# Optimization experiments

Hardware: AMD Instinct MI355X
Metric: run time of the kernel (lower is better)

Reference implementation:

```python
import jax, jax.numpy as jnp
import numpy as np

D_MODEL = 1024


def setup_inputs() -> dict:
    key = jax.random.key(0)
    ks = jax.random.split(key, 7)
    d = D_MODEL
    x = jax.random.normal(ks[0], (4, 2048, d), dtype=jnp.float32)
    scale = 1.0 / np.sqrt(d)
    Wq = jax.random.normal(ks[1], (d, d), dtype=jnp.float32) * scale
    bq = jax.random.normal(ks[2], (d,), dtype=jnp.float32) * 0.01
    Wk = jax.random.normal(ks[3], (d, d), dtype=jnp.float32) * scale
    bk = jax.random.normal(ks[4], (d,), dtype=jnp.float32) * 0.01
    Wo = jax.random.normal(ks[5], (d, 1), dtype=jnp.float32) * scale
    bo = jax.random.normal(ks[6], (1,), dtype=jnp.float32) * 0.01
    return {"x": x, "Wq": Wq, "bq": bq, "Wk": Wk, "bk": bk, "Wo": Wo, "bo": bo}


def reference(x, Wq, bq, Wk, bk, Wo, bo):
    # x: [B, N, d]
    Q = x @ Wq + bq                      # [B, N, d]
    K = x @ Wk + bk                      # [B, N, d]
    scale = x.shape[-1] ** (-0.5)
    content_logits = jnp.einsum('bnd,bmd->bnm', Q, K) * scale  # [B, N, N]
    s = (x @ Wo + bo)[..., 0]            # [B, N]
    # ordering_bias[b, i, j] = tanh(s[b, j] - s[b, i]) * 5
    ordering_bias = jnp.tanh(s[:, None, :] - s[:, :, None]) * 5.0
    return content_logits + ordering_bias
```

## Files before the change

kernel.cpp:

```cpp
#include <hip/hip_runtime.h>
#include <math.h>

#define D_MODEL 1024
#define SEQ 2048
#define NBATCH 4

using bf16x8 = __attribute__((ext_vector_type(8))) short;
using f32x4  = __attribute__((ext_vector_type(4))) float;

__device__ __forceinline__ unsigned short f2bf(float f) {
  union { float f; unsigned int u; } v; v.f = f;
  return (unsigned short)((v.u + 0x7fffu + ((v.u >> 16) & 1u)) >> 16);
}

__device__ __forceinline__ void async_cp16(const void* g, void* l) {
  __builtin_amdgcn_global_load_lds(
      (const __attribute__((address_space(1))) void*)g,
      (__attribute__((address_space(3))) void*)l, 16, 0, 0);
}

__global__ __launch_bounds__(256) void prep_x_kernel(
    const float* __restrict__ x, const float* __restrict__ Wo,
    const float* __restrict__ bo, unsigned short* __restrict__ xb,
    float* __restrict__ tb) {
  const int m = blockIdx.x;
  const int tid = threadIdx.x;
  const float4 xv = ((const float4*)(x + (size_t)m * D_MODEL))[tid];
  const float4 wv = ((const float4*)Wo)[tid];
  ushort4 o;
  o.x = f2bf(xv.x); o.y = f2bf(xv.y); o.z = f2bf(xv.z); o.w = f2bf(xv.w);
  ((ushort4*)(xb + (size_t)m * D_MODEL))[tid] = o;
  float p = xv.x * wv.x + xv.y * wv.y + xv.z * wv.z + xv.w * wv.w;
  #pragma unroll
  for (int off = 32; off > 0; off >>= 1) p += __shfl_down(p, off, 64);
  __shared__ float red[4];
  if ((tid & 63) == 0) red[tid >> 6] = p;
  __syncthreads();
  if (tid == 0) {
    float s = red[0] + red[1] + red[2] + red[3] + bo[0];
    tb[m] = tanhf(s);
  }
}

__global__ __launch_bounds__(256) void prep_w_kernel(
    const float* __restrict__ Wq, const float* __restrict__ Wk,
    unsigned short* __restrict__ WqT, unsigned short* __restrict__ WkT) {
  const float* W = blockIdx.z ? Wk : Wq;
  unsigned short* WT = blockIdx.z ? WkT : WqT;
  const int k0 = blockIdx.y * 32, n0 = blockIdx.x * 32;
  __shared__ unsigned short lds[32][36];
  const int tid = threadIdx.x;
  const int r = tid >> 3, c = (tid & 7) * 4;
  float4 v = *(const float4*)(&W[(size_t)(k0 + r) * D_MODEL + n0 + c]);
  lds[r][c + 0] = f2bf(v.x); lds[r][c + 1] = f2bf(v.y);
  lds[r][c + 2] = f2bf(v.z); lds[r][c + 3] = f2bf(v.w);
  __syncthreads();
  ushort4 o;
  o.x = lds[c + 0][r]; o.y = lds[c + 1][r];
  o.z = lds[c + 2][r]; o.w = lds[c + 3][r];
  *(ushort4*)(&WT[(size_t)(n0 + r) * D_MODEL + k0 + c]) = o;
}

__global__ __launch_bounds__(256) void qkgen_kernel(
    const unsigned short* __restrict__ xb,
    const unsigned short* __restrict__ WqT,
    const unsigned short* __restrict__ WkT,
    const float* __restrict__ bq, const float* __restrict__ bk,
    unsigned short* __restrict__ Qb, unsigned short* __restrict__ Kb) {
  const unsigned short* Bt = blockIdx.z ? WkT : WqT;
  const float* bias = blockIdx.z ? bk : bq;
  unsigned short* Cout = blockIdx.z ? Kb : Qb;
  const int m0 = blockIdx.x * 128;
  const int n0 = blockIdx.y * 128;
  __shared__ unsigned short As[128 * 32];
  __shared__ unsigned short Bs[128 * 32];
  const int tid = threadIdx.x;
  const int lane = tid & 63, w = tid >> 6;
  const int wm = w >> 1, wn = w & 1;
  const int l16 = lane & 15, quad = lane >> 4;

  f32x4 acc[4][4];
  #pragma unroll
  for (int i = 0; i < 4; i++)
    #pragma unroll
    for (int j = 0; j < 4; j++) acc[i][j] = f32x4{0.f, 0.f, 0.f, 0.f};

  const int srow = tid >> 2;
  const int sseg = (tid & 3) * 8;
  const unsigned short* gA = xb + (size_t)(m0 + srow) * D_MODEL + sseg;
  const unsigned short* gB = Bt + (size_t)(n0 + srow) * D_MODEL + sseg;
  unsigned short* lA = As + tid * 8;
  unsigned short* lB = Bs + tid * 8;

  for (int k0 = 0; k0 < D_MODEL; k0 += 32) {
    async_cp16(gA + k0, lA);
    async_cp16(gA + k0 + (size_t)64 * D_MODEL, lA + 2048);
    async_cp16(gB + k0, lB);
    async_cp16(gB + k0 + (size_t)64 * D_MODEL, lB + 2048);
    __syncthreads();
    bf16x8 af[4], bfr[4];
    #pragma unroll
    for (int mt = 0; mt < 4; mt++)
      af[mt] = *(const bf16x8*)(As + (wm * 64 + mt * 16 + l16) * 32 + quad * 8);
    #pragma unroll
    for (int nt = 0; nt < 4; nt++)
      bfr[nt] = *(const bf16x8*)(Bs + (wn * 64 + nt * 16 + l16) * 32 + quad * 8);
    #pragma unroll
    for (int mt = 0; mt < 4; mt++)
      #pragma unroll
      for (int nt = 0; nt < 4; nt++)
        acc[mt][nt] = __builtin_amdgcn_mfma_f32_16x16x32_bf16(
            af[mt], bfr[nt], acc[mt][nt], 0, 0, 0);
    __syncthreads();
  }

  float bv[4];
  #pragma unroll
  for (int nt = 0; nt < 4; nt++) bv[nt] = bias[n0 + wn * 64 + nt * 16 + l16];
  #pragma unroll
  for (int mt = 0; mt < 4; mt++) {
    #pragma unroll
    for (int r = 0; r < 4; r++) {
      const int row = m0 + wm * 64 + mt * 16 + quad * 4 + r;
      unsigned short* cp = Cout + (size_t)row * D_MODEL + n0 + wn * 64 + l16;
      #pragma unroll
      for (int nt = 0; nt < 4; nt++)
        cp[nt * 16] = f2bf(acc[mt][nt][r] + bv[nt]);
    }
  }
}

__global__ __launch_bounds__(256) void qkt_kernel(
    const unsigned short* __restrict__ Qb,
    const unsigned short* __restrict__ Kb,
    const float* __restrict__ tb, float* __restrict__ out) {
  const int b = blockIdx.z;
  const int i0 = blockIdx.x * 128;
  const int j0 = blockIdx.y * 128;
  const unsigned short* A = Qb + (size_t)b * SEQ * D_MODEL;
  const unsigned short* Bt = Kb + (size_t)b * SEQ * D_MODEL;
  __shared__ unsigned short As[128 * 32];
  __shared__ unsigned short Bs[128 * 32];
  __shared__ float tsi[128], tsj[128];
  const int tid = threadIdx.x;
  if (tid < 128) tsi[tid] = tb[b * SEQ + i0 + tid];
  else           tsj[tid - 128] = tb[b * SEQ + j0 + tid - 128];
  const int lane = tid & 63, w = tid >> 6;
  const int wm = w >> 1, wn = w & 1;
  const int l16 = lane & 15, quad = lane >> 4;

  f32x4 acc[4][4];
  #pragma unroll
  for (int i = 0; i < 4; i++)
    #pragma unroll
    for (int j = 0; j < 4; j++) acc[i][j] = f32x4{0.f, 0.f, 0.f, 0.f};

  const int srow = tid >> 2;
  const int sseg = (tid & 3) * 8;
  const unsigned short* gA = A + (size_t)(i0 + srow) * D_MODEL + sseg;
  const unsigned short* gB = Bt + (size_t)(j0 + srow) * D_MODEL + sseg;
  unsigned short* lA = As + tid * 8;
  unsigned short* lB = Bs + tid * 8;

  for (int k0 = 0; k0 < D_MODEL; k0 += 32) {
    async_cp16(gA + k0, lA);
    async_cp16(gA + k0 + (size_t)64 * D_MODEL, lA + 2048);
    async_cp16(gB + k0, lB);
    async_cp16(gB + k0 + (size_t)64 * D_MODEL, lB + 2048);
    __syncthreads();
    bf16x8 af[4], bfr[4];
    #pragma unroll
    for (int mt = 0; mt < 4; mt++)
      af[mt] = *(const bf16x8*)(As + (wm * 64 + mt * 16 + l16) * 32 + quad * 8);
    #pragma unroll
    for (int nt = 0; nt < 4; nt++)
      bfr[nt] = *(const bf16x8*)(Bs + (wn * 64 + nt * 16 + l16) * 32 + quad * 8);
    #pragma unroll
    for (int mt = 0; mt < 4; mt++)
      #pragma unroll
      for (int nt = 0; nt < 4; nt++)
        acc[mt][nt] = __builtin_amdgcn_mfma_f32_16x16x32_bf16(
            af[mt], bfr[nt], acc[mt][nt], 0, 0, 0);
    __syncthreads();
  }

  float tj[4];
  #pragma unroll
  for (int nt = 0; nt < 4; nt++) tj[nt] = tsj[wn * 64 + nt * 16 + l16];
  #pragma unroll
  for (int mt = 0; mt < 4; mt++) {
    #pragma unroll
    for (int r = 0; r < 4; r++) {
      const int il = wm * 64 + mt * 16 + quad * 4 + r;
      const float ti = tsi[il];
      float* cp = out + ((size_t)(b * SEQ + i0 + il)) * SEQ + j0 + wn * 64 + l16;
      #pragma unroll
      for (int nt = 0; nt < 4; nt++) {
        const float num = tj[nt] - ti;
        const float den = fmaf(-tj[nt], ti, 1.0f);
        const float obias = 5.0f * num * __builtin_amdgcn_rcpf(den);
        cp[nt * 16] = 0.03125f * acc[mt][nt][r] + obias;
      }
    }
  }
}

extern "C" void kernel_launch(void* const* d_in, const int* in_sizes, int n_in,
                              void* d_out, int out_size, void* d_ws, size_t ws_size,
                              hipStream_t stream) {
  const float* x  = (const float*)d_in[0];
  const float* Wq = (const float*)d_in[1];
  const float* bq = (const float*)d_in[2];
  const float* Wk = (const float*)d_in[3];
  const float* bk = (const float*)d_in[4];
  const float* Wo = (const float*)d_in[5];
  const float* bo = (const float*)d_in[6];
  float* out = (float*)d_out;

  char* ws = (char*)d_ws;
  unsigned short* xb  = (unsigned short*)(ws);
  unsigned short* WqT = (unsigned short*)(ws + (16ull << 20));
  unsigned short* WkT = (unsigned short*)(ws + (18ull << 20));
  unsigned short* Qb  = (unsigned short*)(ws + (20ull << 20));
  unsigned short* Kb  = (unsigned short*)(ws + (36ull << 20));
  float*          tb  = (float*)(ws + (52ull << 20));

  prep_x_kernel<<<8192, 256, 0, stream>>>(x, Wo, bo, xb, tb);
  prep_w_kernel<<<dim3(32, 32, 2), 256, 0, stream>>>(Wq, Wk, WqT, WkT);
  qkgen_kernel<<<dim3(64, 8, 2), 256, 0, stream>>>(xb, WqT, WkT, bq, bk, Qb, Kb);
  qkt_kernel<<<dim3(16, 16, 4), 256, 0, stream>>>(Qb, Kb, tb, out);
}
```

Before: 203.8 us.

## Double-buffer LDS tiles with k-major layout in both GEMM kernels

```diff
diff --git a/kernel.cpp b/kernel.cpp
--- a/kernel.cpp
+++ b/kernel.cpp
@@ -17,6 +17,16 @@
   __builtin_amdgcn_global_load_lds(
       (const __attribute__((address_space(1))) void*)g,
       (__attribute__((address_space(3))) void*)l, 16, 0, 0);
+}
+
+__device__ __forceinline__ void stage_tile(const unsigned short* gA,
+                                           const unsigned short* gB,
+                                           unsigned short* As,
+                                           unsigned short* Bs, int tid) {
+  async_cp16(gA,      As + tid * 8);
+  async_cp16(gA + 16, As + tid * 8 + 2048);
+  async_cp16(gB,      Bs + tid * 8);
+  async_cp16(gB + 16, Bs + tid * 8 + 2048);
 }
 
 __global__ __launch_bounds__(256) void prep_x_kernel(
@@ -61,7 +71,7 @@
   *(ushort4*)(&WT[(size_t)(n0 + r) * D_MODEL + k0 + c]) = o;
 }
 
-__global__ __launch_bounds__(256) void qkgen_kernel(
+__global__ __launch_bounds__(256, 3) void qkgen_kernel(
     const unsigned short* __restrict__ xb,
     const unsigned short* __restrict__ WqT,
     const unsigned short* __restrict__ WkT,
@@ -72,8 +82,8 @@
   unsigned short* Cout = blockIdx.z ? Kb : Qb;
   const int m0 = blockIdx.x * 128;
   const int n0 = blockIdx.y * 128;
-  __shared__ unsigned short As[128 * 32];
-  __shared__ unsigned short Bs[128 * 32];
+  __shared__ unsigned short As[2][4096];
+  __shared__ unsigned short Bs[2][4096];
   const int tid = threadIdx.x;
   const int lane = tid & 63, w = tid >> 6;
   const int wm = w >> 1, wn = w & 1;
@@ -85,26 +95,27 @@
     #pragma unroll
     for (int j = 0; j < 4; j++) acc[i][j] = f32x4{0.f, 0.f, 0.f, 0.f};
 
-  const int srow = tid >> 2;
-  const int sseg = (tid & 3) * 8;
-  const unsigned short* gA = xb + (size_t)(m0 + srow) * D_MODEL + sseg;
-  const unsigned short* gB = Bt + (size_t)(n0 + srow) * D_MODEL + sseg;
-  unsigned short* lA = As + tid * 8;
-  unsigned short* lB = Bs + tid * 8;
-
-  for (int k0 = 0; k0 < D_MODEL; k0 += 32) {
-    async_cp16(gA + k0, lA);
-    async_cp16(gA + k0 + (size_t)64 * D_MODEL, lA + 2048);
-    async_cp16(gB + k0, lB);
-    async_cp16(gB + k0 + (size_t)64 * D_MODEL, lB + 2048);
-    __syncthreads();
+  const int strow = (w & 1) * 64 + lane;
+  const int stseg = (w >> 1) * 8;
+  const unsigned short* gA = xb + (size_t)(m0 + strow) * D_MODEL + stseg;
+  const unsigned short* gB = Bt + (size_t)(n0 + strow) * D_MODEL + stseg;
+
+  stage_tile(gA, gB, As[0], Bs[0], tid);
+  __syncthreads();
+
+  #pragma unroll 2
+  for (int kk = 0; kk < 32; ++kk) {
+    const int cur = kk & 1;
+    if (kk < 31)
+      stage_tile(gA + (kk + 1) * 32, gB + (kk + 1) * 32,
+                 As[cur ^ 1], Bs[cur ^ 1], tid);
     bf16x8 af[4], bfr[4];
     #pragma unroll
     for (int mt = 0; mt < 4; mt++)
-      af[mt] = *(const bf16x8*)(As + (wm * 64 + mt * 16 + l16) * 32 + quad * 8);
+      af[mt] = *(const bf16x8*)(&As[cur][quad * 1024 + (wm * 64 + mt * 16 + l16) * 8]);
     #pragma unroll
     for (int nt = 0; nt < 4; nt++)
-      bfr[nt] = *(const bf16x8*)(Bs + (wn * 64 + nt * 16 + l16) * 32 + quad * 8);
+      bfr[nt] = *(const bf16x8*)(&Bs[cur][quad * 1024 + (wn * 64 + nt * 16 + l16) * 8]);
     #pragma unroll
     for (int mt = 0; mt < 4; mt++)
       #pragma unroll
@@ -130,7 +141,7 @@
   }
 }
 
-__global__ __launch_bounds__(256) void qkt_kernel(
+__global__ __launch_bounds__(256, 3) void qkt_kernel(
     const unsigned short* __restrict__ Qb,
     const unsigned short* __restrict__ Kb,
     const float* __restrict__ tb, float* __restrict__ out) {
@@ -139,8 +150,8 @@
   const int j0 = blockIdx.y * 128;
   const unsigned short* A = Qb + (size_t)b * SEQ * D_MODEL;
   const unsigned short* Bt = Kb + (size_t)b * SEQ * D_MODEL;
-  __shared__ unsigned short As[128 * 32];
-  __shared__ unsigned short Bs[128 * 32];
+  __shared__ unsigned short As[2][4096];
+  __shared__ unsigned short Bs[2][4096];
   __shared__ float tsi[128], tsj[128];
   const int tid = threadIdx.x;
   if (tid < 128) tsi[tid] = tb[b * SEQ + i0 + tid];
@@ -155,26 +166,27 @@
     #pragma unroll
     for (int j = 0; j < 4; j++) acc[i][j] = f32x4{0.f, 0.f, 0.f, 0.f};
 
-  const int srow = tid >> 2;
-  const int sseg = (tid & 3) * 8;
-  const unsigned short* gA = A + (size_t)(i0 + srow) * D_MODEL + sseg;
-  const unsigned short* gB = Bt + (size_t)(j0 + srow) * D_MODEL + sseg;
-  unsigned short* lA = As + tid * 8;
-  unsigned short* lB = Bs + tid * 8;
-
-  for (int k0 = 0; k0 < D_MODEL; k0 += 32) {
-    async_cp16(gA + k0, lA);
-    async_cp16(gA + k0 + (size_t)64 * D_MODEL, lA + 2048);
-    async_cp16(gB + k0, lB);
-    async_cp16(gB + k0 + (size_t)64 * D_MODEL, lB + 2048);
-    __syncthreads();
+  const int strow = (w & 1) * 64 + lane;
+  const int stseg = (w >> 1) * 8;
+  const unsigned short* gA = A + (size_t)(i0 + strow) * D_MODEL + stseg;
+  const unsigned short* gB = Bt + (size_t)(j0 + strow) * D_MODEL + stseg;
+
+  stage_tile(gA, gB, As[0], Bs[0], tid);
+  __syncthreads();
+
+  #pragma unroll 2
+  for (int kk = 0; kk < 32; ++kk) {
+    const int cur = kk & 1;
+    if (kk < 31)
+      stage_tile(gA + (kk + 1) * 32, gB + (kk + 1) * 32,
+                 As[cur ^ 1], Bs[cur ^ 1], tid);
     bf16x8 af[4], bfr[4];
     #pragma unroll
     for (int mt = 0; mt < 4; mt++)
-      af[mt] = *(const bf16x8*)(As + (wm * 64 + mt * 16 + l16) * 32 + quad * 8);
+      af[mt] = *(const bf16x8*)(&As[cur][quad * 1024 + (wm * 64 + mt * 16 + l16) * 8]);
     #pragma unroll
     for (int nt = 0; nt < 4; nt++)
-      bfr[nt] = *(const bf16x8*)(Bs + (wn * 64 + nt * 16 + l16) * 32 + quad * 8);
+      bfr[nt] = *(const bf16x8*)(&Bs[cur][quad * 1024 + (wn * 64 + nt * 16 + l16) * 8]);
     #pragma unroll
     for (int mt = 0; mt < 4; mt++)
       #pragma unroll
```

Measured after the change: 241.5 us. +18.5%, slower.

## Reassociate QK^T via precomputed Wq·Wk^T and double-buffer swizzled GEMM tiles

Applied to the files above, without the earlier changes.

```diff
diff --git a/kernel.cpp b/kernel.cpp
--- a/kernel.cpp
+++ b/kernel.cpp
@@ -3,7 +3,7 @@
 
 #define D_MODEL 1024
 #define SEQ 2048
-#define NBATCH 4
+#define SCALE 0.03125f
 
 using bf16x8 = __attribute__((ext_vector_type(8))) short;
 using f32x4  = __attribute__((ext_vector_type(4))) float;
@@ -19,187 +19,230 @@
       (__attribute__((address_space(3))) void*)l, 16, 0, 0);
 }
 
-__global__ __launch_bounds__(256) void prep_x_kernel(
-    const float* __restrict__ x, const float* __restrict__ Wo,
-    const float* __restrict__ bo, unsigned short* __restrict__ xb,
-    float* __restrict__ tb) {
-  const int m = blockIdx.x;
-  const int tid = threadIdx.x;
-  const float4 xv = ((const float4*)(x + (size_t)m * D_MODEL))[tid];
-  const float4 wv = ((const float4*)Wo)[tid];
-  ushort4 o;
-  o.x = f2bf(xv.x); o.y = f2bf(xv.y); o.z = f2bf(xv.z); o.w = f2bf(xv.w);
-  ((ushort4*)(xb + (size_t)m * D_MODEL))[tid] = o;
-  float p = xv.x * wv.x + xv.y * wv.y + xv.z * wv.z + xv.w * wv.w;
-  #pragma unroll
-  for (int off = 32; off > 0; off >>= 1) p += __shfl_down(p, off, 64);
-  __shared__ float red[4];
-  if ((tid & 63) == 0) red[tid >> 6] = p;
-  __syncthreads();
-  if (tid == 0) {
-    float s = red[0] + red[1] + red[2] + red[3] + bo[0];
-    tb[m] = tanhf(s);
-  }
-}
-
-__global__ __launch_bounds__(256) void prep_w_kernel(
-    const float* __restrict__ Wq, const float* __restrict__ Wk,
-    unsigned short* __restrict__ WqT, unsigned short* __restrict__ WkT) {
-  const float* W = blockIdx.z ? Wk : Wq;
-  unsigned short* WT = blockIdx.z ? WkT : WqT;
-  const int k0 = blockIdx.y * 32, n0 = blockIdx.x * 32;
-  __shared__ unsigned short lds[32][36];
-  const int tid = threadIdx.x;
-  const int r = tid >> 3, c = (tid & 7) * 4;
-  float4 v = *(const float4*)(&W[(size_t)(k0 + r) * D_MODEL + n0 + c]);
-  lds[r][c + 0] = f2bf(v.x); lds[r][c + 1] = f2bf(v.y);
-  lds[r][c + 2] = f2bf(v.z); lds[r][c + 3] = f2bf(v.w);
-  __syncthreads();
-  ushort4 o;
-  o.x = lds[c + 0][r]; o.y = lds[c + 1][r];
-  o.z = lds[c + 2][r]; o.w = lds[c + 3][r];
-  *(ushort4*)(&WT[(size_t)(n0 + r) * D_MODEL + k0 + c]) = o;
-}
-
-__global__ __launch_bounds__(256) void qkgen_kernel(
-    const unsigned short* __restrict__ xb,
-    const unsigned short* __restrict__ WqT,
-    const unsigned short* __restrict__ WkT,
-    const float* __restrict__ bq, const float* __restrict__ bk,
-    unsigned short* __restrict__ Qb, unsigned short* __restrict__ Kb) {
-  const unsigned short* Bt = blockIdx.z ? WkT : WqT;
-  const float* bias = blockIdx.z ? bk : bq;
-  unsigned short* Cout = blockIdx.z ? Kb : Qb;
-  const int m0 = blockIdx.x * 128;
-  const int n0 = blockIdx.y * 128;
-  __shared__ unsigned short As[128 * 32];
-  __shared__ unsigned short Bs[128 * 32];
-  const int tid = threadIdx.x;
+__device__ __forceinline__ const unsigned short* stage_ptr(
+    const unsigned short* base, int row0, int ld, int tid) {
+  const int r0 = tid >> 2;
+  const int s0 = ((tid & 3) ^ ((r0 >> 1) & 3)) * 8;
+  return base + (size_t)(row0 + r0) * ld + s0;
+}
+
+__device__ __forceinline__ void gemm_core(
+    const unsigned short* __restrict__ gA, const unsigned short* __restrict__ gB,
+    int lda, int ldb, unsigned short* As, unsigned short* Bs, int tid,
+    f32x4 acc[4][4]) {
   const int lane = tid & 63, w = tid >> 6;
   const int wm = w >> 1, wn = w & 1;
   const int l16 = lane & 15, quad = lane >> 4;
 
-  f32x4 acc[4][4];
-  #pragma unroll
-  for (int i = 0; i < 4; i++)
-    #pragma unroll
-    for (int j = 0; j < 4; j++) acc[i][j] = f32x4{0.f, 0.f, 0.f, 0.f};
-
-  const int srow = tid >> 2;
-  const int sseg = (tid & 3) * 8;
-  const unsigned short* gA = xb + (size_t)(m0 + srow) * D_MODEL + sseg;
-  const unsigned short* gB = Bt + (size_t)(n0 + srow) * D_MODEL + sseg;
-  unsigned short* lA = As + tid * 8;
-  unsigned short* lB = Bs + tid * 8;
-
-  for (int k0 = 0; k0 < D_MODEL; k0 += 32) {
-    async_cp16(gA + k0, lA);
-    async_cp16(gA + k0 + (size_t)64 * D_MODEL, lA + 2048);
-    async_cp16(gB + k0, lB);
-    async_cp16(gB + k0 + (size_t)64 * D_MODEL, lB + 2048);
-    __syncthreads();
-    bf16x8 af[4], bfr[4];
-    #pragma unroll
-    for (int mt = 0; mt < 4; mt++)
-      af[mt] = *(const bf16x8*)(As + (wm * 64 + mt * 16 + l16) * 32 + quad * 8);
-    #pragma unroll
-    for (int nt = 0; nt < 4; nt++)
-      bfr[nt] = *(const bf16x8*)(Bs + (wn * 64 + nt * 16 + l16) * 32 + quad * 8);
+  async_cp16(gA,            As + tid * 8);
+  async_cp16(gA + 64 * lda, As + 2048 + tid * 8);
+  async_cp16(gB,            Bs + tid * 8);
+  async_cp16(gB + 64 * ldb, Bs + 2048 + tid * 8);
+  __syncthreads();
+
+  #pragma unroll 2
+  for (int kk = 0; kk < 32; ++kk) {
+    const int cur = (kk & 1) * 4096;
+    const int nxt = 4096 - cur;
+    if (kk < 31) {
+      const unsigned short* a = gA + (kk + 1) * 32;
+      const unsigned short* b = gB + (kk + 1) * 32;
+      async_cp16(a,            As + nxt + tid * 8);
+      async_cp16(a + 64 * lda, As + nxt + 2048 + tid * 8);
+      async_cp16(b,            Bs + nxt + tid * 8);
+      async_cp16(b + 64 * ldb, Bs + nxt + 2048 + tid * 8);
+    }
+    bf16x8 afr[4], bfr[4];
+    #pragma unroll
+    for (int mt = 0; mt < 4; mt++) {
+      const int R = wm * 64 + mt * 16 + l16;
+      afr[mt] = *(const bf16x8*)(As + cur + (R * 4 + (quad ^ ((R >> 1) & 3))) * 8);
+    }
+    #pragma unroll
+    for (int nt = 0; nt < 4; nt++) {
+      const int R = wn * 64 + nt * 16 + l16;
+      bfr[nt] = *(const bf16x8*)(Bs + cur + (R * 4 + (quad ^ ((R >> 1) & 3))) * 8);
+    }
     #pragma unroll
     for (int mt = 0; mt < 4; mt++)
       #pragma unroll
       for (int nt = 0; nt < 4; nt++)
         acc[mt][nt] = __builtin_amdgcn_mfma_f32_16x16x32_bf16(
-            af[mt], bfr[nt], acc[mt][nt], 0, 0, 0);
+            afr[mt], bfr[nt], acc[mt][nt], 0, 0, 0);
     __syncthreads();
   }
-
-  float bv[4];
-  #pragma unroll
-  for (int nt = 0; nt < 4; nt++) bv[nt] = bias[n0 + wn * 64 + nt * 16 + l16];
-  #pragma unroll
-  for (int mt = 0; mt < 4; mt++) {
-    #pragma unroll
-    for (int r = 0; r < 4; r++) {
-      const int row = m0 + wm * 64 + mt * 16 + quad * 4 + r;
-      unsigned short* cp = Cout + (size_t)row * D_MODEL + n0 + wn * 64 + l16;
-      #pragma unroll
-      for (int nt = 0; nt < 4; nt++)
-        cp[nt * 16] = f2bf(acc[mt][nt][r] + bv[nt]);
-    }
-  }
-}
-
-__global__ __launch_bounds__(256) void qkt_kernel(
-    const unsigned short* __restrict__ Qb,
-    const unsigned short* __restrict__ Kb,
-    const float* __restrict__ tb, float* __restrict__ out) {
-  const int b = blockIdx.z;
-  const int i0 = blockIdx.x * 128;
-  const int j0 = blockIdx.y * 128;
-  const unsigned short* A = Qb + (size_t)b * SEQ * D_MODEL;
-  const unsigned short* Bt = Kb + (size_t)b * SEQ * D_MODEL;
-  __shared__ unsigned short As[128 * 32];
-  __shared__ unsigned short Bs[128 * 32];
-  __shared__ float tsi[128], tsj[128];
-  const int tid = threadIdx.x;
-  if (tid < 128) tsi[tid] = tb[b * SEQ + i0 + tid];
-  else           tsj[tid - 128] = tb[b * SEQ + j0 + tid - 128];
+}
+
+__device__ __forceinline__ void store_c_bf16(f32x4 acc[4][4],
+                                             unsigned short* C, int ldc,
+                                             int m0, int n0, int tid) {
   const int lane = tid & 63, w = tid >> 6;
   const int wm = w >> 1, wn = w & 1;
   const int l16 = lane & 15, quad = lane >> 4;
-
+  #pragma unroll
+  for (int mt = 0; mt < 4; mt++) {
+    #pragma unroll
+    for (int r = 0; r < 4; r++) {
+      const int row = m0 + wm * 64 + mt * 16 + quad * 4 + r;
+      unsigned short* cp = C + (size_t)row * ldc + n0 + wn * 64 + l16;
+      #pragma unroll
+      for (int nt = 0; nt < 4; nt++) cp[nt * 16] = f2bf(acc[mt][nt][r]);
+    }
+  }
+}
+
+__global__ __launch_bounds__(256) void wcvt_kernel(
+    const float* __restrict__ Wq, const float* __restrict__ Wk,
+    const float* __restrict__ bq, const float* __restrict__ bk,
+    unsigned short* __restrict__ Wqb, unsigned short* __restrict__ Wkb,
+    float* __restrict__ u, float* __restrict__ v, float* __restrict__ sc) {
+  const int blk = blockIdx.x, tid = threadIdx.x;
+  __shared__ float red[4];
+  float p;
+  if (blk < 2048) {
+    const bool isq = blk < 1024;
+    const int row = blk & 1023;
+    const float* W = isq ? Wq : Wk;
+    const float* bias = isq ? bk : bq;
+    const float4 wv = ((const float4*)(W + (size_t)row * D_MODEL))[tid];
+    const float4 bv = ((const float4*)bias)[tid];
+    ushort4 o;
+    o.x = f2bf(wv.x); o.y = f2bf(wv.y); o.z = f2bf(wv.z); o.w = f2bf(wv.w);
+    ((ushort4*)((isq ? Wqb : Wkb) + (size_t)row * D_MODEL))[tid] = o;
+    p = wv.x * bv.x + wv.y * bv.y + wv.z * bv.z + wv.w * bv.w;
+    #pragma unroll
+    for (int off = 32; off > 0; off >>= 1) p += __shfl_down(p, off, 64);
+    if ((tid & 63) == 0) red[tid >> 6] = p;
+    __syncthreads();
+    if (tid == 0) (isq ? u : v)[row] = red[0] + red[1] + red[2] + red[3];
+  } else {
+    const float4 a = ((const float4*)bq)[tid];
+    const float4 b = ((const float4*)bk)[tid];
+    p = a.x * b.x + a.y * b.y + a.z * b.z + a.w * b.w;
+    #pragma unroll
+    for (int off = 32; off > 0; off >>= 1) p += __shfl_down(p, off, 64);
+    if ((tid & 63) == 0) red[tid >> 6] = p;
+    __syncthreads();
+    if (tid == 0) sc[0] = SCALE * (red[0] + red[1] + red[2] + red[3]);
+  }
+}
+
+__global__ __launch_bounds__(256) void prep_x_kernel(
+    const float* __restrict__ x, const float* __restrict__ Wo,
+    const float* __restrict__ bo, const float* __restrict__ u,
+    const float* __restrict__ v, const float* __restrict__ sc,
+    unsigned short* __restrict__ xb, float* __restrict__ tb,
+    float* __restrict__ aa, float* __restrict__ bb) {
+  const int m = blockIdx.x, tid = threadIdx.x;
+  const float4 xv = ((const float4*)(x + (size_t)m * D_MODEL))[tid];
+  const float4 wv = ((const float4*)Wo)[tid];
+  const float4 uv = ((const float4*)u)[tid];
+  const float4 vv = ((const float4*)v)[tid];
+  ushort4 o;
+  o.x = f2bf(xv.x); o.y = f2bf(xv.y); o.z = f2bf(xv.z); o.w = f2bf(xv.w);
+  ((ushort4*)(xb + (size_t)m * D_MODEL))[tid] = o;
+  float p0 = xv.x * wv.x + xv.y * wv.y + xv.z * wv.z + xv.w * wv.w;
+  float p1 = xv.x * uv.x + xv.y * uv.y + xv.z * uv.z + xv.w * uv.w;
+  float p2 = xv.x * vv.x + xv.y * vv.y + xv.z * vv.z + xv.w * vv.w;
+  #pragma unroll
+  for (int off = 32; off > 0; off >>= 1) {
+    p0 += __shfl_down(p0, off, 64);
+    p1 += __shfl_down(p1, off, 64);
+    p2 += __shfl_down(p2, off, 64);
+  }
+  __shared__ float red[3][4];
+  if ((tid & 63) == 0) {
+    red[0][tid >> 6] = p0; red[1][tid >> 6] = p1; red[2][tid >> 6] = p2;
+  }
+  __syncthreads();
+  if (tid == 0) {
+    tb[m] = tanhf(red[0][0] + red[0][1] + red[0][2] + red[0][3] + bo[0]);
+    aa[m] = SCALE * (red[1][0] + red[1][1] + red[1][2] + red[1][3]) + sc[0];
+    bb[m] = SCALE * (red[2][0] + red[2][1] + red[2][2] + red[2][3]);
+  }
+}
+
+__global__ __launch_bounds__(256, 3) void wmm_kernel(
+    const unsigned short* __restrict__ Wkb,
+    const unsigned short* __restrict__ Wqb, unsigned short* __restrict__ Mt) {
+  const int m0 = blockIdx.x * 128, n0 = blockIdx.y * 128;
+  __shared__ unsigned short As[2 * 4096], Bs[2 * 4096];
+  const int tid = threadIdx.x;
   f32x4 acc[4][4];
   #pragma unroll
   for (int i = 0; i < 4; i++)
     #pragma unroll
     for (int j = 0; j < 4; j++) acc[i][j] = f32x4{0.f, 0.f, 0.f, 0.f};
-
-  const int srow = tid >> 2;
-  const int sseg = (tid & 3) * 8;
-  const unsigned short* gA = A + (size_t)(i0 + srow) * D_MODEL + sseg;
-  const unsigned short* gB = Bt + (size_t)(j0 + srow) * D_MODEL + sseg;
-  unsigned short* lA = As + tid * 8;
-  unsigned short* lB = Bs + tid * 8;
-
-  for (int k0 = 0; k0 < D_MODEL; k0 += 32) {
-    async_cp16(gA + k0, lA);
-    async_cp16(gA + k0 + (size_t)64 * D_MODEL, lA + 2048);
-    async_cp16(gB + k0, lB);
-    async_cp16(gB + k0 + (size_t)64 * D_MODEL, lB + 2048);
-    __syncthreads();
-    bf16x8 af[4], bfr[4];
-    #pragma unroll
-    for (int mt = 0; mt < 4; mt++)
-      af[mt] = *(const bf16x8*)(As + (wm * 64 + mt * 16 + l16) * 32 + quad * 8);
-    #pragma unroll
-    for (int nt = 0; nt < 4; nt++)
-      bfr[nt] = *(const bf16x8*)(Bs + (wn * 64 + nt * 16 + l16) * 32 + quad * 8);
-    #pragma unroll
-    for (int mt = 0; mt < 4; mt++)
-      #pragma unroll
-      for (int nt = 0; nt < 4; nt++)
-        acc[mt][nt] = __builtin_amdgcn_mfma_f32_16x16x32_bf16(
-            af[mt], bfr[nt], acc[mt][nt], 0, 0, 0);
-    __syncthreads();
-  }
-
-  float tj[4];
-  #pragma unroll
-  for (int nt = 0; nt < 4; nt++) tj[nt] = tsj[wn * 64 + nt * 16 + l16];
+  gemm_core(stage_ptr(Wkb, m0, D_MODEL, tid), stage_ptr(Wqb, n0, D_MODEL, tid),
+            D_MODEL, D_MODEL, As, Bs, tid, acc);
+  store_c_bf16(acc, Mt, D_MODEL, m0, n0, tid);
+}
+
+__global__ __launch_bounds__(256, 3) void zgen_kernel(
+    const unsigned short* __restrict__ xb,
+    const unsigned short* __restrict__ Mt, unsigned short* __restrict__ Zb) {
+  const int m0 = blockIdx.x * 128, n0 = blockIdx.y * 128;
+  __shared__ unsigned short As[2 * 4096], Bs[2 * 4096];
+  const int tid = threadIdx.x;
+  f32x4 acc[4][4];
+  #pragma unroll
+  for (int i = 0; i < 4; i++)
+    #pragma unroll
+    for (int j = 0; j < 4; j++) acc[i][j] = f32x4{0.f, 0.f, 0.f, 0.f};
+  gemm_core(stage_ptr(xb, m0, D_MODEL, tid), stage_ptr(Mt, n0, D_MODEL, tid),
+            D_MODEL, D_MODEL, As, Bs, tid, acc);
+  store_c_bf16(acc, Zb, D_MODEL, m0, n0, tid);
+}
+
+__global__ __launch_bounds__(256, 3) void zxt_kernel(
+    const unsigned short* __restrict__ Zb, const unsigned short* __restrict__ xb,
+    const float* __restrict__ tb, const float* __restrict__ aa,
+    const float* __restrict__ bb, float* __restrict__ out) {
+  const int b = blockIdx.z;
+  const int i0 = blockIdx.x * 128, j0 = blockIdx.y * 128;
+  __shared__ unsigned short As[2 * 4096], Bs[2 * 4096];
+  __shared__ float tsi[128], tsj[128], tsa[128], tsb[128];
+  const int tid = threadIdx.x;
+  if (tid < 128) {
+    tsi[tid] = tb[b * SEQ + i0 + tid];
+    tsa[tid] = aa[b * SEQ + i0 + tid];
+  } else {
+    tsj[tid - 128] = tb[b * SEQ + j0 + tid - 128];
+    tsb[tid - 128] = bb[b * SEQ + j0 + tid - 128];
+  }
+  f32x4 acc[4][4];
+  #pragma unroll
+  for (int i = 0; i < 4; i++)
+    #pragma unroll
+    for (int j = 0; j < 4; j++) acc[i][j] = f32x4{0.f, 0.f, 0.f, 0.f};
+  const unsigned short* A = Zb + (size_t)b * SEQ * D_MODEL;
+  const unsigned short* Bt = xb + (size_t)b * SEQ * D_MODEL;
+  gemm_core(stage_ptr(A, i0, D_MODEL, tid), stage_ptr(Bt, j0, D_MODEL, tid),
+            D_MODEL, D_MODEL, As, Bs, tid, acc);
+
+  const int lane = tid & 63, w = tid >> 6;
+  const int wm = w >> 1, wn = w & 1;
+  const int l16 = lane & 15, quad = lane >> 4;
+  float tj[4], bj[4];
+  #pragma unroll
+  for (int nt = 0; nt < 4; nt++) {
+    tj[nt] = tsj[wn * 64 + nt * 16 + l16];
+    bj[nt] = tsb[wn * 64 + nt * 16 + l16];
+  }
   #pragma unroll
   for (int mt = 0; mt < 4; mt++) {
     #pragma unroll
     for (int r = 0; r < 4; r++) {
       const int il = wm * 64 + mt * 16 + quad * 4 + r;
       const float ti = tsi[il];
+      const float ai = tsa[il];
       float* cp = out + ((size_t)(b * SEQ + i0 + il)) * SEQ + j0 + wn * 64 + l16;
       #pragma unroll
       for (int nt = 0; nt < 4; nt++) {
         const float num = tj[nt] - ti;
         const float den = fmaf(-tj[nt], ti, 1.0f);
         const float obias = 5.0f * num * __builtin_amdgcn_rcpf(den);
-        cp[nt * 16] = 0.03125f * acc[mt][nt][r] + obias;
+        cp[nt * 16] = SCALE * acc[mt][nt][r] + ai + bj[nt] + obias;
       }
     }
   }
@@ -219,14 +262,20 @@
 
   char* ws = (char*)d_ws;
   unsigned short* xb  = (unsigned short*)(ws);
-  unsigned short* WqT = (unsigned short*)(ws + (16ull << 20));
-  unsigned short* WkT = (unsigned short*)(ws + (18ull << 20));
-  unsigned short* Qb  = (unsigned short*)(ws + (20ull << 20));
-  unsigned short* Kb  = (unsigned short*)(ws + (36ull << 20));
-  float*          tb  = (float*)(ws + (52ull << 20));
-
-  prep_x_kernel<<<8192, 256, 0, stream>>>(x, Wo, bo, xb, tb);
-  prep_w_kernel<<<dim3(32, 32, 2), 256, 0, stream>>>(Wq, Wk, WqT, WkT);
-  qkgen_kernel<<<dim3(64, 8, 2), 256, 0, stream>>>(xb, WqT, WkT, bq, bk, Qb, Kb);
-  qkt_kernel<<<dim3(16, 16, 4), 256, 0, stream>>>(Qb, Kb, tb, out);
-}
+  unsigned short* Zb  = (unsigned short*)(ws + (16ull << 20));
+  unsigned short* Wqb = (unsigned short*)(ws + (32ull << 20));
+  unsigned short* Wkb = (unsigned short*)(ws + (34ull << 20));
+  unsigned short* Mt  = (unsigned short*)(ws + (36ull << 20));
+  float* tb = (float*)(ws + (38ull << 20));
+  float* aa = (float*)(ws + (38ull << 20) + (32ull << 10));
+  float* bb = (float*)(ws + (38ull << 20) + (64ull << 10));
+  float* u  = (float*)(ws + (38ull << 20) + (96ull << 10));
+  float* v  = (float*)(ws + (38ull << 20) + (100ull << 10));
+  float* sc = (float*)(ws + (38ull << 20) + (104ull << 10));
+
+  wcvt_kernel<<<2049, 256, 0, stream>>>(Wq, Wk, bq, bk, Wqb, Wkb, u, v, sc);
+  prep_x_kernel<<<8192, 256, 0, stream>>>(x, Wo, bo, u, v, sc, xb, tb, aa, bb);
+  wmm_kernel<<<dim3(8, 8), 256, 0, stream>>>(Wkb, Wqb, Mt);
+  zgen_kernel<<<dim3(64, 8), 256, 0, stream>>>(xb, Mt, Zb);
+  zxt_kernel<<<dim3(16, 16, 4), 256, 0, stream>>>(Zb, xb, tb, aa, bb, out);
+}
```

Result: faster. 195.2 us (-4.2%).
